# Kernel tuning notes

Hardware: AMD Instinct MI355X
Metric: run time of the kernel (lower is better)

## Reference

```python
import jax, jax.numpy as jnp
import numpy as np

TEMPERATURE = 0.07
EPS = 1e-12  # matches torch F.normalize default eps


def setup_inputs() -> dict:
    key = jax.random.key(0)
    k1, k2 = jax.random.split(key)
    N, D = 8192, 1024
    return {
        "query": jax.random.normal(k1, (N, D), dtype=jnp.float32),
        "key": jax.random.normal(k2, (N, D), dtype=jnp.float32),
    }


def _l2_normalize(x):
    norm = jnp.sqrt(jnp.sum(x * x, axis=-1, keepdims=True))
    return x / jnp.maximum(norm, EPS)


def reference(query, key):
    q = _l2_normalize(query)            # [N, D]
    k = _l2_normalize(key)              # [N, D]
    logits = jnp.einsum("nd,md->nm", q, k) / TEMPERATURE  # [N, N]
    # cross-entropy with diagonal labels = mean(logsumexp(row) - diag)
    diag = jnp.diagonal(logits)
    fwd_loss = jnp.mean(jax.nn.logsumexp(logits, axis=1) - diag)
    bwd_loss = jnp.mean(jax.nn.logsumexp(logits, axis=0) - diag)
    return 0.5 * (fwd_loss + bwd_loss)
```

## Files before the change

### kernel.cpp

```cpp
#include <hip/hip_runtime.h>
#include <math.h>

#define N 8192
#define D 1024
#define INV_T 14.285714285714286f

typedef unsigned short ushortT;
typedef unsigned int uintT;
typedef __bf16 bf16x8 __attribute__((ext_vector_type(8)));
typedef float f32x4 __attribute__((ext_vector_type(4)));

#define AS1 __attribute__((address_space(1)))
#define AS3 __attribute__((address_space(3)))

__device__ __forceinline__ ushortT f2bf(float x) {
    uintT u = __float_as_uint(x);
    return (ushortT)((u + 0x7fffu + ((u >> 16) & 1u)) >> 16);
}

__global__ __launch_bounds__(256)
void normalize_bf16_kernel(const float* __restrict__ q, const float* __restrict__ k,
                           ushortT* __restrict__ qh, ushortT* __restrict__ kh,
                           float* __restrict__ diag,
                           float* __restrict__ rowsum, float* __restrict__ colsum,
                           float* __restrict__ out) {
    const int row = blockIdx.x;
    const int tid = threadIdx.x;
    if (tid == 64) rowsum[row] = 0.f;
    if (tid == 65) colsum[row] = 0.f;
    if (row == 0 && tid == 66) out[0] = INV_T;

    const float4 a = *(const float4*)(q + (size_t)row * D + tid * 4);
    const float4 b = *(const float4*)(k + (size_t)row * D + tid * 4);
    float sqq = a.x*a.x + a.y*a.y + a.z*a.z + a.w*a.w;
    float skk = b.x*b.x + b.y*b.y + b.z*b.z + b.w*b.w;
    float sqk = a.x*b.x + a.y*b.y + a.z*b.z + a.w*b.w;
    #pragma unroll
    for (int m = 1; m < 64; m <<= 1) {
        sqq += __shfl_xor(sqq, m, 64);
        skk += __shfl_xor(skk, m, 64);
        sqk += __shfl_xor(sqk, m, 64);
    }
    __shared__ float red[3][4];
    __shared__ float s_iq, s_ik;
    const int wid = tid >> 6, lane = tid & 63;
    if (lane == 0) { red[0][wid] = sqq; red[1][wid] = skk; red[2][wid] = sqk; }
    __syncthreads();
    if (tid == 0) {
        float s0 = red[0][0] + red[0][1] + red[0][2] + red[0][3];
        float s1 = red[1][0] + red[1][1] + red[1][2] + red[1][3];
        float s2 = red[2][0] + red[2][1] + red[2][2] + red[2][3];
        float iq = 1.0f / fmaxf(sqrtf(s0), 1e-12f);
        float ik = 1.0f / fmaxf(sqrtf(s1), 1e-12f);
        s_iq = iq; s_ik = ik;
        diag[row] = s2 * iq * ik * INV_T;
    }
    __syncthreads();
    const float iq = s_iq, ik = s_ik;

    const size_t base = (size_t)row * D + tid * 4;
    float av[4] = {a.x * iq, a.y * iq, a.z * iq, a.w * iq};
    float bv[4] = {b.x * ik, b.y * ik, b.z * ik, b.w * ik};
    ushort4 qv, kv;
    ushortT* qp = (ushortT*)&qv; ushortT* kp = (ushortT*)&kv;
    #pragma unroll
    for (int j = 0; j < 4; ++j) { qp[j] = f2bf(av[j]); kp[j] = f2bf(bv[j]); }
    *(ushort4*)(qh + base) = qv;
    *(ushort4*)(kh + base) = kv;
}

#define LBUF 65536
#define NT 16

__global__ __launch_bounds__(512, 2)
void mfma256_lse_kernel(const ushortT* __restrict__ qh, const ushortT* __restrict__ kh,
                        float* __restrict__ rowsum, float* __restrict__ colsum) {
    __shared__ __align__(16) char lds[2 * LBUF];

    const int wg  = blockIdx.x;
    const int swz = (wg & 7) * 128 + (wg >> 3);
    const int bi  = swz >> 5;
    const int bj  = swz & 31;

    const int tid  = threadIdx.x;
    const int w    = tid >> 6;
    const int lane = tid & 63;
    const int wm   = w >> 2, wn = w & 3;
    const int la   = lane & 15, lq = lane >> 4;

    size_t aoff[4], boff[4];
    int dstb[4];
    #pragma unroll
    for (int i = 0; i < 4; ++i) {
        int lin = i * 512 + tid;
        int r   = lin >> 3;
        int s   = lin & 7;
        int sp  = s ^ (r & 7);
        aoff[i] = (size_t)(bi * 256 + r) * D + sp * 8;
        boff[i] = (size_t)(bj * 256 + r) * D + sp * 8;
        dstb[i] = lin * 16;
    }

    int byteA[8][2], byteB[4][2];
    #pragma unroll
    for (int f = 0; f < 8; ++f) {
        int ra = wm * 128 + f * 16 + la;
        byteA[f][0] = ra * 128 + ((lq       ^ (ra & 7)) * 16);
        byteA[f][1] = ra * 128 + (((lq ^ 4) ^ (ra & 7)) * 16);
    }
    #pragma unroll
    for (int n = 0; n < 4; ++n) {
        int rb = wn * 64 + n * 16 + la;
        byteB[n][0] = 32768 + rb * 128 + ((lq       ^ (rb & 7)) * 16);
        byteB[n][1] = 32768 + rb * 128 + (((lq ^ 4) ^ (rb & 7)) * 16);
    }

    f32x4 acc[8][4] = {};

#define STAGE(t1) do { \
    char* db_ = lds + (((t1) & 1) * LBUF); \
    const size_t kof_ = (size_t)(t1) * 64; \
    _Pragma("unroll") \
    for (int i_ = 0; i_ < 4; ++i_) { \
        __builtin_amdgcn_global_load_lds( \
            (const AS1 void*)(qh + aoff[i_] + kof_), \
            (AS3 void*)(db_ + dstb[i_]), 16, 0, 0); \
        __builtin_amdgcn_global_load_lds( \
            (const AS1 void*)(kh + boff[i_] + kof_), \
            (AS3 void*)(db_ + 32768 + dstb[i_]), 16, 0, 0); \
    } } while (0)

    STAGE(0);
    asm volatile("s_waitcnt vmcnt(0)" ::: "memory");
    __builtin_amdgcn_s_barrier();

    #pragma unroll 1
    for (int t = 0; t < NT; ++t) {
        const char* bufb = lds + (t & 1) * LBUF;

        if (t < NT - 1) STAGE(t + 1);

        bf16x8 bF[4][2];
        #pragma unroll
        for (int n = 0; n < 4; ++n) {
            bF[n][0] = *(const bf16x8*)(bufb + byteB[n][0]);
            bF[n][1] = *(const bf16x8*)(bufb + byteB[n][1]);
        }

        {
            bf16x8 aF[4][2];
            #pragma unroll
            for (int f = 0; f < 4; ++f) {
                aF[f][0] = *(const bf16x8*)(bufb + byteA[f][0]);
                aF[f][1] = *(const bf16x8*)(bufb + byteA[f][1]);
            }
            __builtin_amdgcn_s_setprio(1);
            #pragma unroll
            for (int f = 0; f < 4; ++f)
                #pragma unroll
                for (int n = 0; n < 4; ++n) {
                    acc[f][n] = __builtin_amdgcn_mfma_f32_16x16x32_bf16(aF[f][0], bF[n][0], acc[f][n], 0, 0, 0);
                    acc[f][n] = __builtin_amdgcn_mfma_f32_16x16x32_bf16(aF[f][1], bF[n][1], acc[f][n], 0, 0, 0);
                }
            __builtin_amdgcn_s_setprio(0);
        }
        __builtin_amdgcn_s_barrier();

        {
            bf16x8 aF[4][2];
            #pragma unroll
            for (int f = 0; f < 4; ++f) {
                aF[f][0] = *(const bf16x8*)(bufb + byteA[f + 4][0]);
                aF[f][1] = *(const bf16x8*)(bufb + byteA[f + 4][1]);
            }
            __builtin_amdgcn_s_setprio(1);
            #pragma unroll
            for (int f = 0; f < 4; ++f)
                #pragma unroll
                for (int n = 0; n < 4; ++n) {
                    acc[f + 4][n] = __builtin_amdgcn_mfma_f32_16x16x32_bf16(aF[f][0], bF[n][0], acc[f + 4][n], 0, 0, 0);
                    acc[f + 4][n] = __builtin_amdgcn_mfma_f32_16x16x32_bf16(aF[f][1], bF[n][1], acc[f + 4][n], 0, 0, 0);
                }
            __builtin_amdgcn_s_setprio(0);
        }
        __syncthreads();
    }
#undef STAGE

    #pragma unroll
    for (int f = 0; f < 8; ++f)
        #pragma unroll
        for (int n = 0; n < 4; ++n)
            #pragma unroll
            for (int r = 0; r < 4; ++r)
                acc[f][n][r] = __expf((acc[f][n][r] - 1.0f) * INV_T);

    #pragma unroll
    for (int f = 0; f < 8; ++f)
        #pragma unroll
        for (int r = 0; r < 4; ++r) {
            float v = acc[f][0][r] + acc[f][1][r] + acc[f][2][r] + acc[f][3][r];
            v += __shfl_xor(v, 1, 64);
            v += __shfl_xor(v, 2, 64);
            v += __shfl_xor(v, 4, 64);
            v += __shfl_xor(v, 8, 64);
            if (la == 0)
                atomicAdd(&rowsum[bi * 256 + wm * 128 + f * 16 + lq * 4 + r], v);
        }

    #pragma unroll
    for (int n = 0; n < 4; ++n) {
        float v = 0.f;
        #pragma unroll
        for (int f = 0; f < 8; ++f)
            #pragma unroll
            for (int r = 0; r < 4; ++r)
                v += acc[f][n][r];
        v += __shfl_xor(v, 16, 64);
        v += __shfl_xor(v, 32, 64);
        if (lq == 0)
            atomicAdd(&colsum[bj * 256 + wn * 64 + n * 16 + la], v);
    }
}

__global__ __launch_bounds__(1024)
void final_kernel(const float* __restrict__ rowsum, const float* __restrict__ colsum,
                  const float* __restrict__ diag, float* __restrict__ out) {
    const int tid = threadIdx.x;
    const int i = blockIdx.x * 1024 + tid;
    float p = 0.5f * (logf(rowsum[i]) + logf(colsum[i])) - diag[i];
    #pragma unroll
    for (int m = 1; m < 64; m <<= 1) p += __shfl_xor(p, m, 64);
    __shared__ float red[16];
    const int wid = tid >> 6, lane = tid & 63;
    if (lane == 0) red[wid] = p;
    __syncthreads();
    if (tid == 0) {
        float t = 0.f;
        #pragma unroll
        for (int w = 0; w < 16; ++w) t += red[w];
        atomicAdd(out, t / (float)N);
    }
}

#define BT 128
__global__ __launch_bounds__(256)
void norms_diag_kernel(const float* __restrict__ q, const float* __restrict__ k,
                       float* __restrict__ invq, float* __restrict__ invk,
                       float* __restrict__ diag, float* __restrict__ out) {
    const int row = blockIdx.x;
    const int tid = threadIdx.x;
    if (row == 0 && tid == 66) out[0] = INV_T;
    float4 a = *(const float4*)(q + (size_t)row * D + tid * 4);
    float4 b = *(const float4*)(k + (size_t)row * D + tid * 4);
    float sqq = a.x*a.x + a.y*a.y + a.z*a.z + a.w*a.w;
    float skk = b.x*b.x + b.y*b.y + b.z*b.z + b.w*b.w;
    float sqk = a.x*b.x + a.y*b.y + a.z*b.z + a.w*b.w;
    #pragma unroll
    for (int m = 1; m < 64; m <<= 1) {
        sqq += __shfl_xor(sqq, m, 64);
        skk += __shfl_xor(skk, m, 64);
        sqk += __shfl_xor(sqk, m, 64);
    }
    __shared__ float red[3][4];
    const int wid = tid >> 6, lane = tid & 63;
    if (lane == 0) { red[0][wid] = sqq; red[1][wid] = skk; red[2][wid] = sqk; }
    __syncthreads();
    if (tid == 0) {
        float s0 = red[0][0] + red[0][1] + red[0][2] + red[0][3];
        float s1 = red[1][0] + red[1][1] + red[1][2] + red[1][3];
        float s2 = red[2][0] + red[2][1] + red[2][2] + red[2][3];
        float iq = 1.0f / fmaxf(sqrtf(s0), 1e-12f);
        float ik = 1.0f / fmaxf(sqrtf(s1), 1e-12f);
        invq[row] = iq; invk[row] = ik;
        diag[row] = s2 * iq * ik * INV_T;
    }
}

#define KBF 16
#define LDTF 132
__global__ __launch_bounds__(256)
void gemm_lse_kernel(const float* __restrict__ q, const float* __restrict__ k,
                     const float* __restrict__ invq, const float* __restrict__ invk,
                     float* __restrict__ rowsum, float* __restrict__ colsum) {
    __shared__ float As[KBF * LDTF];
    __shared__ float Bs[KBF * LDTF];
    const int tid = threadIdx.x;
    const int tx = tid & 15;
    const int ty = tid >> 4;
    const int bi = blockIdx.y;
    const int bj = blockIdx.x;
    const float* qb = q + (size_t)(bi * BT) * D;
    const float* kb = k + (size_t)(bj * BT) * D;
    float acc[8][8] = {};
    for (int k0 = 0; k0 < D; k0 += KBF) {
        #pragma unroll
        for (int i = 0; i < 2; ++i) {
            int idx  = tid + i * 256;
            int row  = idx >> 2;
            int kc4  = idx & 3;
            float4 av = *(const float4*)(qb + (size_t)row * D + k0 + kc4 * 4);
            float4 bv = *(const float4*)(kb + (size_t)row * D + k0 + kc4 * 4);
            int base = (kc4 * 4) * LDTF + row;
            As[base] = av.x; As[base + LDTF] = av.y; As[base + 2*LDTF] = av.z; As[base + 3*LDTF] = av.w;
            Bs[base] = bv.x; Bs[base + LDTF] = bv.y; Bs[base + 2*LDTF] = bv.z; Bs[base + 3*LDTF] = bv.w;
        }
        __syncthreads();
        #pragma unroll
        for (int kk = 0; kk < KBF; ++kk) {
            const float* ap = &As[kk * LDTF + ty * 8];
            const float* bp = &Bs[kk * LDTF + tx * 8];
            float4 a0 = *(const float4*)(ap);
            float4 a1 = *(const float4*)(ap + 4);
            float4 b0 = *(const float4*)(bp);
            float4 b1 = *(const float4*)(bp + 4);
            float ar[8] = {a0.x, a0.y, a0.z, a0.w, a1.x, a1.y, a1.z, a1.w};
            float br[8] = {b0.x, b0.y, b0.z, b0.w, b1.x, b1.y, b1.z, b1.w};
            #pragma unroll
            for (int r = 0; r < 8; ++r)
                #pragma unroll
                for (int c = 0; c < 8; ++c)
                    acc[r][c] += ar[r] * br[c];
        }
        __syncthreads();
    }
    float iqr[8], ikc[8];
    #pragma unroll
    for (int r = 0; r < 8; ++r) iqr[r] = invq[bi * BT + ty * 8 + r] * INV_T;
    #pragma unroll
    for (int c = 0; c < 8; ++c) ikc[c] = invk[bj * BT + tx * 8 + c];
    float rowpart[8] = {};
    float colpart[8] = {};
    #pragma unroll
    for (int r = 0; r < 8; ++r)
        #pragma unroll
        for (int c = 0; c < 8; ++c) {
            float e = __expf(acc[r][c] * iqr[r] * ikc[c] - INV_T);
            rowpart[r] += e; colpart[c] += e;
        }
    #pragma unroll
    for (int r = 0; r < 8; ++r) {
        float v = rowpart[r];
        v += __shfl_xor(v, 1, 64); v += __shfl_xor(v, 2, 64);
        v += __shfl_xor(v, 4, 64); v += __shfl_xor(v, 8, 64);
        if (tx == 0) atomicAdd(&rowsum[bi * BT + ty * 8 + r], v);
    }
    __syncthreads();
    float* colbuf = As;
    #pragma unroll
    for (int c = 0; c < 8; ++c) colbuf[ty * 128 + tx * 8 + c] = colpart[c];
    __syncthreads();
    if (tid < 128) {
        float s = 0.f;
        #pragma unroll
        for (int t2 = 0; t2 < 16; ++t2) s += colbuf[t2 * 128 + tid];
        atomicAdd(&colsum[bj * BT + tid], s);
    }
}

extern "C" void kernel_launch(void* const* d_in, const int* in_sizes, int n_in,
                              void* d_out, int out_size, void* d_ws, size_t ws_size,
                              hipStream_t stream) {
    const float* q = (const float*)d_in[0];
    const float* k = (const float*)d_in[1];

    const size_t planeBytes = 2ull * N * D * sizeof(ushortT);
    const size_t needFast   = planeBytes + 3ull * N * sizeof(float);

    if (ws_size >= needFast) {
        ushortT* qh = (ushortT*)d_ws;
        ushortT* kh = qh + (size_t)N * D;
        float* tail  = (float*)((char*)d_ws + planeBytes);
        float* rowsum = tail;
        float* colsum = tail + N;
        float* diag   = tail + 2 * N;

        normalize_bf16_kernel<<<N, 256, 0, stream>>>(q, k, qh, kh, diag,
                                                     rowsum, colsum, (float*)d_out);
        mfma256_lse_kernel<<<(N / 256) * (N / 256), 512, 0, stream>>>(qh, kh, rowsum, colsum);
        final_kernel<<<N / 1024, 1024, 0, stream>>>(rowsum, colsum, diag, (float*)d_out);
    } else {
        float* ws     = (float*)d_ws;
        float* invq   = ws;
        float* invk   = ws + N;
        float* rowsum = ws + 2 * N;
        float* colsum = ws + 3 * N;
        float* diag   = ws + 4 * N;
        hipMemsetAsync(rowsum, 0, 2ull * N * sizeof(float), stream);
        norms_diag_kernel<<<N, 256, 0, stream>>>(q, k, invq, invk, diag, (float*)d_out);
        gemm_lse_kernel<<<dim3(N / BT, N / BT), 256, 0, stream>>>(q, k, invq, invk, rowsum, colsum);
        final_kernel<<<N / 1024, 1024, 0, stream>>>(rowsum, colsum, diag, (float*)d_out);
    }
}
```

Measured before the change: 296.7 us.

## Process one row per wavefront in normalize and split MFMA loop into barrier-interleaved phases

```diff
diff --git a/kernel.cpp b/kernel.cpp
--- a/kernel.cpp
+++ b/kernel.cpp
@@ -24,49 +24,49 @@
                            float* __restrict__ diag,
                            float* __restrict__ rowsum, float* __restrict__ colsum,
                            float* __restrict__ out) {
-    const int row = blockIdx.x;
-    const int tid = threadIdx.x;
-    if (tid == 64) rowsum[row] = 0.f;
-    if (tid == 65) colsum[row] = 0.f;
-    if (row == 0 && tid == 66) out[0] = INV_T;
-
-    const float4 a = *(const float4*)(q + (size_t)row * D + tid * 4);
-    const float4 b = *(const float4*)(k + (size_t)row * D + tid * 4);
-    float sqq = a.x*a.x + a.y*a.y + a.z*a.z + a.w*a.w;
-    float skk = b.x*b.x + b.y*b.y + b.z*b.z + b.w*b.w;
-    float sqk = a.x*b.x + a.y*b.y + a.z*b.z + a.w*b.w;
+    const int wid  = threadIdx.x >> 6;
+    const int lane = threadIdx.x & 63;
+    const int row  = blockIdx.x * 4 + wid;
+    if (lane == 60) rowsum[row] = 0.f;
+    if (lane == 61) colsum[row] = 0.f;
+    if (row == 0 && lane == 62) out[0] = INV_T;
+
+    const float* qr = q + (size_t)row * D;
+    const float* kr = k + (size_t)row * D;
+    float4 a[4], b[4];
+    #pragma unroll
+    for (int j = 0; j < 4; ++j) {
+        a[j] = *(const float4*)(qr + j * 256 + lane * 4);
+        b[j] = *(const float4*)(kr + j * 256 + lane * 4);
+    }
+    float sqq = 0.f, skk = 0.f, sqk = 0.f;
+    #pragma unroll
+    for (int j = 0; j < 4; ++j) {
+        sqq += a[j].x*a[j].x + a[j].y*a[j].y + a[j].z*a[j].z + a[j].w*a[j].w;
+        skk += b[j].x*b[j].x + b[j].y*b[j].y + b[j].z*b[j].z + b[j].w*b[j].w;
+        sqk += a[j].x*b[j].x + a[j].y*b[j].y + a[j].z*b[j].z + a[j].w*b[j].w;
+    }
     #pragma unroll
     for (int m = 1; m < 64; m <<= 1) {
         sqq += __shfl_xor(sqq, m, 64);
         skk += __shfl_xor(skk, m, 64);
         sqk += __shfl_xor(sqk, m, 64);
     }
-    __shared__ float red[3][4];
-    __shared__ float s_iq, s_ik;
-    const int wid = tid >> 6, lane = tid & 63;
-    if (lane == 0) { red[0][wid] = sqq; red[1][wid] = skk; red[2][wid] = sqk; }
-    __syncthreads();
-    if (tid == 0) {
-        float s0 = red[0][0] + red[0][1] + red[0][2] + red[0][3];
-        float s1 = red[1][0] + red[1][1] + red[1][2] + red[1][3];
-        float s2 = red[2][0] + red[2][1] + red[2][2] + red[2][3];
-        float iq = 1.0f / fmaxf(sqrtf(s0), 1e-12f);
-        float ik = 1.0f / fmaxf(sqrtf(s1), 1e-12f);
-        s_iq = iq; s_ik = ik;
-        diag[row] = s2 * iq * ik * INV_T;
-    }
-    __syncthreads();
-    const float iq = s_iq, ik = s_ik;
-
-    const size_t base = (size_t)row * D + tid * 4;
-    float av[4] = {a.x * iq, a.y * iq, a.z * iq, a.w * iq};
-    float bv[4] = {b.x * ik, b.y * ik, b.z * ik, b.w * ik};
-    ushort4 qv, kv;
-    ushortT* qp = (ushortT*)&qv; ushortT* kp = (ushortT*)&kv;
-    #pragma unroll
-    for (int j = 0; j < 4; ++j) { qp[j] = f2bf(av[j]); kp[j] = f2bf(bv[j]); }
-    *(ushort4*)(qh + base) = qv;
-    *(ushort4*)(kh + base) = kv;
+    const float iq = 1.0f / fmaxf(sqrtf(sqq), 1e-12f);
+    const float ik = 1.0f / fmaxf(sqrtf(skk), 1e-12f);
+    if (lane == 0) diag[row] = sqk * iq * ik * INV_T;
+
+    #pragma unroll
+    for (int j = 0; j < 4; ++j) {
+        float av[4] = {a[j].x * iq, a[j].y * iq, a[j].z * iq, a[j].w * iq};
+        float bv[4] = {b[j].x * ik, b[j].y * ik, b[j].z * ik, b[j].w * ik};
+        ushort4 qv, kv;
+        ushortT* qp = (ushortT*)&qv; ushortT* kp = (ushortT*)&kv;
+        #pragma unroll
+        for (int e = 0; e < 4; ++e) { qp[e] = f2bf(av[e]); kp[e] = f2bf(bv[e]); }
+        *(ushort4*)(qh + (size_t)row * D + j * 256 + lane * 4) = qv;
+        *(ushort4*)(kh + (size_t)row * D + j * 256 + lane * 4) = kv;
+    }
 }
 
 #define LBUF 65536
@@ -130,9 +130,11 @@
             (AS3 void*)(db_ + 32768 + dstb[i_]), 16, 0, 0); \
     } } while (0)
 
+#define BAR() __builtin_amdgcn_s_barrier()
+
     STAGE(0);
     asm volatile("s_waitcnt vmcnt(0)" ::: "memory");
-    __builtin_amdgcn_s_barrier();
+    BAR();
 
     #pragma unroll 1
     for (int t = 0; t < NT; ++t) {
@@ -140,52 +142,63 @@
 
         if (t < NT - 1) STAGE(t + 1);
 
-        bf16x8 bF[4][2];
-        #pragma unroll
-        for (int n = 0; n < 4; ++n) {
-            bF[n][0] = *(const bf16x8*)(bufb + byteB[n][0]);
-            bF[n][1] = *(const bf16x8*)(bufb + byteB[n][1]);
-        }
-
-        {
-            bf16x8 aF[4][2];
-            #pragma unroll
-            for (int f = 0; f < 4; ++f) {
-                aF[f][0] = *(const bf16x8*)(bufb + byteA[f][0]);
-                aF[f][1] = *(const bf16x8*)(bufb + byteA[f][1]);
-            }
-            __builtin_amdgcn_s_setprio(1);
-            #pragma unroll
-            for (int f = 0; f < 4; ++f)
-                #pragma unroll
-                for (int n = 0; n < 4; ++n) {
-                    acc[f][n] = __builtin_amdgcn_mfma_f32_16x16x32_bf16(aF[f][0], bF[n][0], acc[f][n], 0, 0, 0);
-                    acc[f][n] = __builtin_amdgcn_mfma_f32_16x16x32_bf16(aF[f][1], bF[n][1], acc[f][n], 0, 0, 0);
-                }
-            __builtin_amdgcn_s_setprio(0);
-        }
-        __builtin_amdgcn_s_barrier();
-
-        {
-            bf16x8 aF[4][2];
-            #pragma unroll
-            for (int f = 0; f < 4; ++f) {
-                aF[f][0] = *(const bf16x8*)(bufb + byteA[f + 4][0]);
-                aF[f][1] = *(const bf16x8*)(bufb + byteA[f + 4][1]);
-            }
-            __builtin_amdgcn_s_setprio(1);
-            #pragma unroll
-            for (int f = 0; f < 4; ++f)
-                #pragma unroll
-                for (int n = 0; n < 4; ++n) {
-                    acc[f + 4][n] = __builtin_amdgcn_mfma_f32_16x16x32_bf16(aF[f][0], bF[n][0], acc[f + 4][n], 0, 0, 0);
-                    acc[f + 4][n] = __builtin_amdgcn_mfma_f32_16x16x32_bf16(aF[f][1], bF[n][1], acc[f + 4][n], 0, 0, 0);
-                }
-            __builtin_amdgcn_s_setprio(0);
-        }
-        __syncthreads();
+        bf16x8 bk[4], aF[4];
+
+        #pragma unroll
+        for (int n = 0; n < 4; ++n) bk[n] = *(const bf16x8*)(bufb + byteB[n][0]);
+        #pragma unroll
+        for (int f = 0; f < 4; ++f) aF[f] = *(const bf16x8*)(bufb + byteA[f][0]);
+        BAR();
+        __builtin_amdgcn_s_setprio(1);
+        #pragma unroll
+        for (int f = 0; f < 4; ++f)
+            #pragma unroll
+            for (int n = 0; n < 4; ++n)
+                acc[f][n] = __builtin_amdgcn_mfma_f32_16x16x32_bf16(aF[f], bk[n], acc[f][n], 0, 0, 0);
+        __builtin_amdgcn_s_setprio(0);
+        BAR();
+
+        #pragma unroll
+        for (int f = 0; f < 4; ++f) aF[f] = *(const bf16x8*)(bufb + byteA[f + 4][0]);
+        BAR();
+        __builtin_amdgcn_s_setprio(1);
+        #pragma unroll
+        for (int f = 0; f < 4; ++f)
+            #pragma unroll
+            for (int n = 0; n < 4; ++n)
+                acc[f + 4][n] = __builtin_amdgcn_mfma_f32_16x16x32_bf16(aF[f], bk[n], acc[f + 4][n], 0, 0, 0);
+        __builtin_amdgcn_s_setprio(0);
+        BAR();
+
+        #pragma unroll
+        for (int n = 0; n < 4; ++n) bk[n] = *(const bf16x8*)(bufb + byteB[n][1]);
+        #pragma unroll
+        for (int f = 0; f < 4; ++f) aF[f] = *(const bf16x8*)(bufb + byteA[f][1]);
+        BAR();
+        __builtin_amdgcn_s_setprio(1);
+        #pragma unroll
+        for (int f = 0; f < 4; ++f)
+            #pragma unroll
+            for (int n = 0; n < 4; ++n)
+                acc[f][n] = __builtin_amdgcn_mfma_f32_16x16x32_bf16(aF[f], bk[n], acc[f][n], 0, 0, 0);
+        __builtin_amdgcn_s_setprio(0);
+        BAR();
+
+        #pragma unroll
+        for (int f = 0; f < 4; ++f) aF[f] = *(const bf16x8*)(bufb + byteA[f + 4][1]);
+        BAR();
+        __builtin_amdgcn_s_setprio(1);
+        #pragma unroll
+        for (int f = 0; f < 4; ++f)
+            #pragma unroll
+            for (int n = 0; n < 4; ++n)
+                acc[f + 4][n] = __builtin_amdgcn_mfma_f32_16x16x32_bf16(aF[f], bk[n], acc[f + 4][n], 0, 0, 0);
+        __builtin_amdgcn_s_setprio(0);
+        asm volatile("s_waitcnt vmcnt(0)" ::: "memory");
+        BAR();
     }
 #undef STAGE
+#undef BAR
 
     #pragma unroll
     for (int f = 0; f < 8; ++f)
@@ -375,8 +388,8 @@
         float* colsum = tail + N;
         float* diag   = tail + 2 * N;
 
-        normalize_bf16_kernel<<<N, 256, 0, stream>>>(q, k, qh, kh, diag,
-                                                     rowsum, colsum, (float*)d_out);
+        normalize_bf16_kernel<<<N / 4, 256, 0, stream>>>(q, k, qh, kh, diag,
+                                                         rowsum, colsum, (float*)d_out);
         mfma256_lse_kernel<<<(N / 256) * (N / 256), 512, 0, stream>>>(qh, kh, rowsum, colsum);
         final_kernel<<<N / 1024, 1024, 0, stream>>>(rowsum, colsum, diag, (float*)d_out);
     } else {
```

After: 297.7 us. Within noise of the previous version (+0.3%).
